# Performance work log

Measured on AMD Instinct MI355X. Metric: run time of the kernel, lower is better.

Reference implementation:

```python
import jax, jax.numpy as jnp
import numpy as np

HID = 128  # args['hidden_size']


def preprocess_adj(A):
    # A: [B, N, N] -> D^{-1/2} (A + I) D^{-1/2}
    N = A.shape[1]
    A_hat = A + jnp.eye(N, dtype=A.dtype)
    d = jnp.sum(A_hat, axis=2)                     # [B, N]
    d_safe = jnp.where(d > 0, d, 1.0)
    d_inv = jnp.where(d > 0, d_safe ** -0.5, 0.0)  # inf -> 0, as in torch code
    return d_inv[:, :, None] * A_hat * d_inv[:, None, :]


def lstm(x, w_ih, w_hh, b_ih, b_hh):
    # x: [B, T, H]; PyTorch gate order i, f, g, o; zero init state
    B = x.shape[0]
    H = w_hh.shape[1]
    def step(carry, xt):
        h, c = carry
        z = xt @ w_ih.T + b_ih + h @ w_hh.T + b_hh
        i, f, g, o = jnp.split(z, 4, axis=-1)
        c = jax.nn.sigmoid(f) * c + jax.nn.sigmoid(i) * jnp.tanh(g)
        h = jax.nn.sigmoid(o) * jnp.tanh(c)
        return (h, c), h
    h0 = jnp.zeros((B, H), x.dtype)
    c0 = jnp.zeros((B, H), x.dtype)
    _, hs = jax.lax.scan(step, (h0, c0), jnp.swapaxes(x, 0, 1))
    return jnp.swapaxes(hs, 0, 1)  # [B, T, H]


def gcn_dynamic_forward(x, A_norm, conv_w, conv_b, w_ih, w_hh, b_ih, b_hh):
    # x: [B, N, HID] with N >= HID: take last HID rows as dynamic-filter input
    df_in = x[:, x.shape[1] - HID:, :]              # [B, HID, HID]
    dyn = jax.lax.conv_general_dilated(
        df_in, conv_w, window_strides=(1,), padding=[(1, 1)],
        dimension_numbers=('NCH', 'OIH', 'NCH')) + conv_b[None, :, None]
    lw = lstm(dyn, w_ih, w_hh, b_ih, b_hh)          # [B, HID, HID]
    agg = jnp.matmul(A_norm, x)                     # [B, N, HID]
    out = jax.nn.sigmoid(jnp.matmul(agg, lw))       # output activation (1-layer GCN)
    return out                                       # dropout is identity in eval


def setup_inputs() -> dict:
    key = jax.random.key(0)
    ks = jax.random.split(key, 8)
    B, N = 4, 4096
    node_embedding = jax.random.normal(ks[0], (B, N, HID), dtype=jnp.float32)
    # sparse symmetric-ish 0/1 adjacency, avg degree ~ N*0.01
    adjacency_matrix = (jax.random.uniform(ks[1], (B, N, N)) < 0.01).astype(jnp.float32)
    s = 0.05
    conv_w = jax.random.normal(ks[2], (HID, HID, 3), dtype=jnp.float32) * s
    conv_b = jax.random.normal(ks[3], (HID,), dtype=jnp.float32) * s
    w_ih = jax.random.normal(ks[4], (4 * HID, HID), dtype=jnp.float32) * s
    w_hh = jax.random.normal(ks[5], (4 * HID, HID), dtype=jnp.float32) * s
    b_ih = jax.random.normal(ks[6], (4 * HID,), dtype=jnp.float32) * s
    b_hh = jax.random.normal(ks[7], (4 * HID,), dtype=jnp.float32) * s
    return {"node_embedding": node_embedding, "adjacency_matrix": adjacency_matrix,
            "conv_w": conv_w, "conv_b": conv_b,
            "w_ih": w_ih, "w_hh": w_hh, "b_ih": b_ih, "b_hh": b_hh}


def reference(node_embedding, adjacency_matrix, conv_w, conv_b, w_ih, w_hh, b_ih, b_hh):
    A_norm = preprocess_adj(adjacency_matrix)
    return gcn_dynamic_forward(node_embedding, A_norm, conv_w, conv_b, w_ih, w_hh, b_ih, b_hh)
```

## Files before the change

kernel.cpp:

```cpp
#include <hip/hip_runtime.h>
#include <math.h>

#define N_NODES 4096
#define HIDN 128
#define MAXNZ 128

typedef float v4f __attribute__((ext_vector_type(4)));
typedef _Float16 h2 __attribute__((ext_vector_type(2)));
typedef _Float16 h8 __attribute__((ext_vector_type(8)));

__device__ __forceinline__ float fsig(float x) { return 1.0f / (1.0f + __expf(-x)); }
__device__ __forceinline__ float ftanh_(float x) { return 1.0f - 2.0f / (__expf(2.0f * x) + 1.0f); }

__global__ __launch_bounds__(512) void k_conv(
        const float* __restrict__ x, const float* __restrict__ conv_w,
        const float* __restrict__ conv_b, const float* __restrict__ w_ih,
        const float* __restrict__ b_ih, const float* __restrict__ b_hh,
        float* __restrict__ z3) {
    const int cb = blockIdx.x;
    const int b = cb >> 5;
    const int t0 = (cb & 31) * 4;
    const int tsub = threadIdx.x >> 7;
    const int h = threadIdx.x & 127;
    const int t = t0 + tsub;
    __shared__ __align__(16) float dyn_lds[4][HIDN];
    const float* xb = x + ((size_t)b * N_NODES + (N_NODES - HIDN)) * HIDN;
    const float* w = conv_w + (size_t)t * HIDN * 3;
    float a0 = conv_b[t], a1 = 0.0f, a2 = 0.0f, a3 = 0.0f;
    #pragma unroll 4
    for (int i = 0; i < HIDN; i += 4) {
        const float* xr0 = xb + (size_t)i * HIDN;
        #pragma unroll
        for (int s = 0; s < 4; ++s) {
            const float* xr = xr0 + s * HIDN;
            float w0 = w[(i + s) * 3 + 0], w1 = w[(i + s) * 3 + 1], w2 = w[(i + s) * 3 + 2];
            float left  = (h > 0)   ? xr[h - 1] : 0.0f;
            float mid   = xr[h];
            float right = (h < 127) ? xr[h + 1] : 0.0f;
            if (s == 0)      a0 += left * w0 + mid * w1 + right * w2;
            else if (s == 1) a1 += left * w0 + mid * w1 + right * w2;
            else if (s == 2) a2 += left * w0 + mid * w1 + right * w2;
            else             a3 += left * w0 + mid * w1 + right * w2;
        }
    }
    dyn_lds[tsub][h] = (a0 + a1) + (a2 + a3);
    __syncthreads();
    const float4* dyn4 = (const float4*)dyn_lds[tsub];
    float* zrow = z3 + (size_t)(b * HIDN + t) * 512;
    for (int qg = 0; qg < 4; ++qg) {
        int u = h + 128 * qg;
        const float4* wr = (const float4*)(w_ih + (size_t)u * HIDN);
        float za = b_ih[u] + b_hh[u];
        #pragma unroll
        for (int f4 = 0; f4 < 32; ++f4) {
            float4 wv = wr[f4];
            float4 dv = dyn4[f4];
            za += wv.x * dv.x + wv.y * dv.y + wv.z * dv.z + wv.w * dv.w;
        }
        zrow[h * 4 + qg] = za;
    }
}

__global__ __launch_bounds__(512, 2) void k_lstm_scan(
        const float* __restrict__ z3, const float* __restrict__ w_hh,
        float* __restrict__ lw,
        const float* __restrict__ A, float* __restrict__ d_inv,
        int* __restrict__ cnt, int* __restrict__ idx) {
    if (blockIdx.x < 4) {
        const int b = blockIdx.x;
        const int t = threadIdx.x;
        const int m = t >> 2;
        const int q = t & 3;
        __shared__ __align__(16) h2 hbuf[2][64];
        h2 w2[4][16];
        #pragma unroll
        for (int g = 0; g < 4; ++g) {
            const float4* wr = (const float4*)(w_hh + ((size_t)(g * HIDN + m)) * HIDN + q * 32);
            #pragma unroll
            for (int j4 = 0; j4 < 8; ++j4) {
                float4 wv = wr[j4];
                w2[g][2 * j4 + 0] = h2{(_Float16)wv.x, (_Float16)wv.y};
                w2[g][2 * j4 + 1] = h2{(_Float16)wv.z, (_Float16)wv.w};
            }
        }
        float c = 0.0f;
        if (t < 64) hbuf[0][t] = h2{(_Float16)0.0f, (_Float16)0.0f};
        const float4* zb = (const float4*)z3 + (size_t)b * HIDN * HIDN;
        float4 zc = zb[0 * HIDN + m];
        float4 zn = zb[1 * HIDN + m];
        __syncthreads();
        for (int s = 0; s < HIDN; ++s) {
            const h8* hq8 = ((const h8*)hbuf[s & 1]) + q * 4;
            h8 H0 = hq8[0], H1 = hq8[1], H2 = hq8[2], H3 = hq8[3];
            const h2* hp = (const h2*)&H0;
            h2 hh[16];
            #pragma unroll
            for (int j = 0; j < 4; ++j) {
                hh[j]      = ((const h2*)&H0)[j];
                hh[4 + j]  = ((const h2*)&H1)[j];
                hh[8 + j]  = ((const h2*)&H2)[j];
                hh[12 + j] = ((const h2*)&H3)[j];
            }
            (void)hp;
            float s0a = 0.f, s0b = 0.f, s1a = 0.f, s1b = 0.f;
            float s2a = 0.f, s2b = 0.f, s3a = 0.f, s3b = 0.f;
            #pragma unroll
            for (int j = 0; j < 8; ++j) {
                s0a = __builtin_amdgcn_fdot2(w2[0][2 * j], hh[2 * j], s0a, false);
                s0b = __builtin_amdgcn_fdot2(w2[0][2 * j + 1], hh[2 * j + 1], s0b, false);
                s1a = __builtin_amdgcn_fdot2(w2[1][2 * j], hh[2 * j], s1a, false);
                s1b = __builtin_amdgcn_fdot2(w2[1][2 * j + 1], hh[2 * j + 1], s1b, false);
                s2a = __builtin_amdgcn_fdot2(w2[2][2 * j], hh[2 * j], s2a, false);
                s2b = __builtin_amdgcn_fdot2(w2[2][2 * j + 1], hh[2 * j + 1], s2b, false);
                s3a = __builtin_amdgcn_fdot2(w2[3][2 * j], hh[2 * j], s3a, false);
                s3b = __builtin_amdgcn_fdot2(w2[3][2 * j + 1], hh[2 * j + 1], s3b, false);
            }
            float z0 = s0a + s0b, z1 = s1a + s1b, z2 = s2a + s2b, z3s = s3a + s3b;
            z0 += __shfl_xor(z0, 1); z0 += __shfl_xor(z0, 2);
            z1 += __shfl_xor(z1, 1); z1 += __shfl_xor(z1, 2);
            z2 += __shfl_xor(z2, 1); z2 += __shfl_xor(z2, 2);
            z3s += __shfl_xor(z3s, 1); z3s += __shfl_xor(z3s, 2);
            z0 += zc.x; z1 += zc.y; z2 += zc.z; z3s += zc.w;
            float ig = fsig(z0);
            float fg = fsig(z1);
            float gg = ftanh_(z2);
            float og = fsig(z3s);
            c = fg * c + ig * gg;
            float hn = og * ftanh_(c);
            if (q == 0) {
                ((_Float16*)hbuf[(s + 1) & 1])[m] = (_Float16)hn;
                lw[(size_t)(b * HIDN + s) * HIDN + m] = hn;
            }
            zc = zn;
            int s2n = (s + 2 < HIDN) ? (s + 2) : (HIDN - 1);
            zn = zb[(size_t)s2n * HIDN + m];
            __syncthreads();
        }
    } else {
        const int wid = threadIdx.x >> 6;
        const int lane = threadIdx.x & 63;
        const int r = (blockIdx.x - 4) * 8 + wid;
        const v4f* row = (const v4f*)(A + (size_t)r * N_NODES);
        int* idx_row = idx + r * MAXNZ;
        const unsigned long long below = (1ull << lane) - 1ull;
        int cbase = 0;
#define PROC1(c, col)                                                         \
        {                                                                     \
            bool nz = ((c) != 0.0f);                                          \
            unsigned long long mm = __ballot(nz);                             \
            if (mm) {                                                         \
                if (nz) {                                                     \
                    int p_ = cbase + __popcll(mm & below);                    \
                    if (p_ < MAXNZ) idx_row[p_] = (col);                      \
                }                                                             \
                cbase += __popcll(mm);                                        \
            }                                                                 \
        }
        for (int half = 0; half < 2; ++half) {
            v4f v[8];
            #pragma unroll
            for (int j = 0; j < 8; ++j)
                v[j] = __builtin_nontemporal_load(&row[half * 512 + j * 64 + lane]);
            #pragma unroll
            for (int j = 0; j < 8; ++j) {
                int col0 = (half * 512 + j * 64 + lane) * 4;
                PROC1(v[j].x, col0 + 0);
                PROC1(v[j].y, col0 + 1);
                PROC1(v[j].z, col0 + 2);
                PROC1(v[j].w, col0 + 3);
            }
        }
#undef PROC1
        if (lane == 0) {
            cnt[r] = (cbase < MAXNZ) ? cbase : MAXNZ;
            d_inv[r] = rsqrtf((float)(cbase + 1));
        }
    }
}

__global__ __launch_bounds__(512) void k_gather(
        const float* __restrict__ x, const float* __restrict__ d_inv,
        const int* __restrict__ cnt, const int* __restrict__ idx,
        float* __restrict__ agg) {
    const int bIdx = blockIdx.x;
    const int b = (bIdx & 7) >> 1;
    const int o = ((bIdx >> 3) << 1) | (bIdx & 1);
    const int wid = threadIdx.x >> 6;
    const int lane = threadIdx.x & 63;
    __shared__ __align__(16) float dl[N_NODES];
    {
        const float4* dsrc = (const float4*)(d_inv + (b << 12));
        float4* ddst = (float4*)dl;
        ddst[threadIdx.x] = dsrc[threadIdx.x];
        ddst[threadIdx.x + 512] = dsrc[threadIdx.x + 512];
    }
    __syncthreads();
    const int i = o * 8 + wid;
    const int r = (b << 12) + i;
    const float2* xb = (const float2*)(x + (size_t)b * N_NODES * HIDN);
    const int4* irow4 = (const int4*)(idx + r * MAXNZ);
    const int n = cnt[r];
    float ax = 0.0f, ay = 0.0f;
    int k = 0;
    if (n >= 4) {
        int4 cur = irow4[0];
        for (; k + 4 <= n; k += 4) {
            int4 nxt = (k + 8 <= n) ? irow4[(k >> 2) + 1] : cur;
            float d0 = dl[cur.x], d1 = dl[cur.y], d2 = dl[cur.z], d3 = dl[cur.w];
            float2 v0 = xb[(size_t)cur.x * 64 + lane];
            float2 v1 = xb[(size_t)cur.y * 64 + lane];
            float2 v2 = xb[(size_t)cur.z * 64 + lane];
            float2 v3 = xb[(size_t)cur.w * 64 + lane];
            ax += d0 * v0.x + d1 * v1.x + d2 * v2.x + d3 * v3.x;
            ay += d0 * v0.y + d1 * v1.y + d2 * v2.y + d3 * v3.y;
            cur = nxt;
        }
    }
    const int* irow = (const int*)irow4;
    for (; k < n; ++k) {
        int j = irow[k];
        float dj = dl[j];
        float2 v = xb[(size_t)j * 64 + lane];
        ax += dj * v.x;
        ay += dj * v.y;
    }
    float di = dl[i];
    float2 vi = xb[(size_t)i * 64 + lane];
    float2 out;
    out.x = di * (ax + di * vi.x);
    out.y = di * (ay + di * vi.y);
    ((float2*)(agg + (size_t)r * HIDN))[lane] = out;
}

__global__ __launch_bounds__(256) void k_outmm(
        const float* __restrict__ agg, const float* __restrict__ lw,
        float* __restrict__ out) {
    __shared__ __align__(16) float lw_lds[HIDN * HIDN];
    const int i0 = blockIdx.x * 64;
    const int b = i0 >> 12;
    const float4* lwg = (const float4*)(lw + (size_t)b * HIDN * HIDN);
    float4* lds4 = (float4*)lw_lds;
    for (int v = threadIdx.x; v < HIDN * HIDN / 4; v += 256) lds4[v] = lwg[v];
    __syncthreads();
    const int r0 = i0 + (threadIdx.x >> 3) * 2;
    const int u0 = (threadIdx.x & 7) * 16;
    const float4* a4 = (const float4*)agg;
    float4 acc[2][4];
    #pragma unroll
    for (int rr = 0; rr < 2; ++rr)
        #pragma unroll
        for (int cc = 0; cc < 4; ++cc) acc[rr][cc] = make_float4(0.f, 0.f, 0.f, 0.f);
    for (int f4 = 0; f4 < 32; ++f4) {
        float4 a0 = a4[(size_t)r0 * 32 + f4];
        float4 a1 = a4[(size_t)(r0 + 1) * 32 + f4];
        #pragma unroll
        for (int ff = 0; ff < 4; ++ff) {
            float af0 = (ff == 0) ? a0.x : (ff == 1) ? a0.y : (ff == 2) ? a0.z : a0.w;
            float af1 = (ff == 0) ? a1.x : (ff == 1) ? a1.y : (ff == 2) ? a1.z : a1.w;
            int f = f4 * 4 + ff;
            const float4* wrow = (const float4*)(lw_lds + f * HIDN + u0);
            #pragma unroll
            for (int cc = 0; cc < 4; ++cc) {
                float4 wv = wrow[cc];
                acc[0][cc].x += af0 * wv.x; acc[0][cc].y += af0 * wv.y;
                acc[0][cc].z += af0 * wv.z; acc[0][cc].w += af0 * wv.w;
                acc[1][cc].x += af1 * wv.x; acc[1][cc].y += af1 * wv.y;
                acc[1][cc].z += af1 * wv.z; acc[1][cc].w += af1 * wv.w;
            }
        }
    }
    #pragma unroll
    for (int rr = 0; rr < 2; ++rr) {
        #pragma unroll
        for (int cc = 0; cc < 4; ++cc) {
            float4 ov;
            ov.x = fsig(acc[rr][cc].x);
            ov.y = fsig(acc[rr][cc].y);
            ov.z = fsig(acc[rr][cc].z);
            ov.w = fsig(acc[rr][cc].w);
            *(float4*)(out + (size_t)(r0 + rr) * HIDN + u0 + cc * 4) = ov;
        }
    }
}

extern "C" void kernel_launch(void* const* d_in, const int* in_sizes, int n_in,
                              void* d_out, int out_size, void* d_ws, size_t ws_size,
                              hipStream_t stream) {
    const float* x      = (const float*)d_in[0];
    const float* A      = (const float*)d_in[1];
    const float* conv_w = (const float*)d_in[2];
    const float* conv_b = (const float*)d_in[3];
    const float* w_ih   = (const float*)d_in[4];
    const float* w_hh   = (const float*)d_in[5];
    const float* b_ih   = (const float*)d_in[6];
    const float* b_hh   = (const float*)d_in[7];
    float* out = (float*)d_out;

    char* ws = (char*)d_ws;
    float* d_inv = (float*)ws;
    int*   cnt   = (int*)(ws + 65536);
    int*   idx   = (int*)(ws + 131072);
    float* z3    = (float*)(ws + 131072 + 8388608);
    float* lw    = (float*)(ws + 131072 + 8388608 + 1048576);
    float* agg   = (float*)(ws + 131072 + 8388608 + 1048576 + 262144);

    hipLaunchKernelGGL(k_conv, dim3(128), dim3(512), 0, stream,
                       x, conv_w, conv_b, w_ih, b_ih, b_hh, z3);
    hipLaunchKernelGGL(k_lstm_scan, dim3(2052), dim3(512), 0, stream,
                       z3, w_hh, lw, A, d_inv, cnt, idx);
    hipLaunchKernelGGL(k_gather, dim3(2048), dim3(512), 0, stream,
                       x, d_inv, cnt, idx, agg);
    hipLaunchKernelGGL(k_outmm, dim3(256), dim3(256), 0, stream, agg, lw, out);
}
```

Before: 573.2 us.

## Split LSTM and adjacency scan into separate kernels, chunk gate-input layout

Splits the combined kernel that ran the LSTM recurrence alongside the adjacency nonzero scan into two launches: k_scan, then k_lstm. The gate pre-activations are stored in 16-step chunks, so each thread loads its inputs per chunk with vector loads. Each thread folds its own gate input into a dot-product accumulator, and hidden states are buffered and written per chunk rather than every step. The gather kernel moves to 256-thread blocks with an 8-wide unrolled neighbour loop, and the scan drops its nontemporal loads. The cost is that the serial LSTM no longer overlaps the bandwidth-bound adjacency scan, so its latency lands on the critical path.

Result: slower. 606.9 us (+5.9%).

```diff
diff --git a/kernel.cpp b/kernel.cpp
--- a/kernel.cpp
+++ b/kernel.cpp
@@ -16,7 +16,7 @@
         const float* __restrict__ x, const float* __restrict__ conv_w,
         const float* __restrict__ conv_b, const float* __restrict__ w_ih,
         const float* __restrict__ b_ih, const float* __restrict__ b_hh,
-        float* __restrict__ z3) {
+        float* __restrict__ z4) {
     const int cb = blockIdx.x;
     const int b = cb >> 5;
     const int t0 = (cb & 31) * 4;
@@ -46,7 +46,7 @@
     dyn_lds[tsub][h] = (a0 + a1) + (a2 + a3);
     __syncthreads();
     const float4* dyn4 = (const float4*)dyn_lds[tsub];
-    float* zrow = z3 + (size_t)(b * HIDN + t) * 512;
+    const int ch = t >> 4, si = t & 15;
     for (int qg = 0; qg < 4; ++qg) {
         int u = h + 128 * qg;
         const float4* wr = (const float4*)(w_ih + (size_t)u * HIDN);
@@ -57,42 +57,86 @@
             float4 dv = dyn4[f4];
             za += wv.x * dv.x + wv.y * dv.y + wv.z * dv.z + wv.w * dv.w;
         }
-        zrow[h * 4 + qg] = za;
-    }
-}
-
-__global__ __launch_bounds__(512, 2) void k_lstm_scan(
-        const float* __restrict__ z3, const float* __restrict__ w_hh,
-        float* __restrict__ lw,
+        z4[(((size_t)(b * 8 + ch) * 128 + h) * 4 + qg) * 16 + si] = za;
+    }
+}
+
+__global__ __launch_bounds__(256) void k_scan(
         const float* __restrict__ A, float* __restrict__ d_inv,
         int* __restrict__ cnt, int* __restrict__ idx) {
-    if (blockIdx.x < 4) {
-        const int b = blockIdx.x;
-        const int t = threadIdx.x;
-        const int m = t >> 2;
-        const int q = t & 3;
-        __shared__ __align__(16) h2 hbuf[2][64];
-        h2 w2[4][16];
-        #pragma unroll
-        for (int g = 0; g < 4; ++g) {
-            const float4* wr = (const float4*)(w_hh + ((size_t)(g * HIDN + m)) * HIDN + q * 32);
-            #pragma unroll
-            for (int j4 = 0; j4 < 8; ++j4) {
-                float4 wv = wr[j4];
-                w2[g][2 * j4 + 0] = h2{(_Float16)wv.x, (_Float16)wv.y};
-                w2[g][2 * j4 + 1] = h2{(_Float16)wv.z, (_Float16)wv.w};
-            }
-        }
-        float c = 0.0f;
-        if (t < 64) hbuf[0][t] = h2{(_Float16)0.0f, (_Float16)0.0f};
-        const float4* zb = (const float4*)z3 + (size_t)b * HIDN * HIDN;
-        float4 zc = zb[0 * HIDN + m];
-        float4 zn = zb[1 * HIDN + m];
-        __syncthreads();
-        for (int s = 0; s < HIDN; ++s) {
+    const int wid = threadIdx.x >> 6;
+    const int lane = threadIdx.x & 63;
+    const int r = blockIdx.x * 4 + wid;
+    const v4f* row = (const v4f*)(A + (size_t)r * N_NODES);
+    int* idx_row = idx + r * MAXNZ;
+    const unsigned long long below = (1ull << lane) - 1ull;
+    int cbase = 0;
+#define PROC1(c, col)                                                         \
+    {                                                                         \
+        bool nz = ((c) != 0.0f);                                              \
+        unsigned long long mm = __ballot(nz);                                 \
+        if (mm) {                                                             \
+            if (nz) {                                                         \
+                int p_ = cbase + __popcll(mm & below);                        \
+                if (p_ < MAXNZ) idx_row[p_] = (col);                          \
+            }                                                                 \
+            cbase += __popcll(mm);                                            \
+        }                                                                     \
+    }
+    for (int half = 0; half < 2; ++half) {
+        v4f v[8];
+        #pragma unroll
+        for (int j = 0; j < 8; ++j)
+            v[j] = row[half * 512 + j * 64 + lane];
+        #pragma unroll
+        for (int j = 0; j < 8; ++j) {
+            int col0 = (half * 512 + j * 64 + lane) * 4;
+            PROC1(v[j].x, col0 + 0);
+            PROC1(v[j].y, col0 + 1);
+            PROC1(v[j].z, col0 + 2);
+            PROC1(v[j].w, col0 + 3);
+        }
+    }
+#undef PROC1
+    if (lane == 0) {
+        cnt[r] = (cbase < MAXNZ) ? cbase : MAXNZ;
+        d_inv[r] = rsqrtf((float)(cbase + 1));
+    }
+}
+
+__global__ __launch_bounds__(512) void k_lstm(
+        const float* __restrict__ z4, const float* __restrict__ w_hh,
+        float* __restrict__ lw) {
+    const int b = blockIdx.x;
+    const int t = threadIdx.x;
+    const int m = t >> 2;
+    const int q = t & 3;
+    __shared__ __align__(16) h2 hbuf[2][64];
+    h2 w2[4][16];
+    #pragma unroll
+    for (int g = 0; g < 4; ++g) {
+        const float4* wr = (const float4*)(w_hh + ((size_t)(g * HIDN + m)) * HIDN + q * 32);
+        #pragma unroll
+        for (int j4 = 0; j4 < 8; ++j4) {
+            float4 wv = wr[j4];
+            w2[g][2 * j4 + 0] = h2{(_Float16)wv.x, (_Float16)wv.y};
+            w2[g][2 * j4 + 1] = h2{(_Float16)wv.z, (_Float16)wv.w};
+        }
+    }
+    float c = 0.0f;
+    if (t < 64) hbuf[0][t] = h2{(_Float16)0.0f, (_Float16)0.0f};
+    __syncthreads();
+    for (int ch = 0; ch < 8; ++ch) {
+        const float4* zc = (const float4*)(z4 + ((((size_t)(b * 8 + ch) * 128 + m) * 4 + q) * 16));
+        float4 zr0 = zc[0], zr1 = zc[1], zr2 = zc[2], zr3 = zc[3];
+        float zs[16] = {zr0.x, zr0.y, zr0.z, zr0.w, zr1.x, zr1.y, zr1.z, zr1.w,
+                        zr2.x, zr2.y, zr2.z, zr2.w, zr3.x, zr3.y, zr3.z, zr3.w};
+        float hist[16];
+        #pragma unroll
+        for (int si = 0; si < 16; ++si) {
+            const int s = ch * 16 + si;
             const h8* hq8 = ((const h8*)hbuf[s & 1]) + q * 4;
             h8 H0 = hq8[0], H1 = hq8[1], H2 = hq8[2], H3 = hq8[3];
-            const h2* hp = (const h2*)&H0;
             h2 hh[16];
             #pragma unroll
             for (int j = 0; j < 4; ++j) {
@@ -101,84 +145,50 @@
                 hh[8 + j]  = ((const h2*)&H2)[j];
                 hh[12 + j] = ((const h2*)&H3)[j];
             }
-            (void)hp;
-            float s0a = 0.f, s0b = 0.f, s1a = 0.f, s1b = 0.f;
-            float s2a = 0.f, s2b = 0.f, s3a = 0.f, s3b = 0.f;
+            float zq = zs[si];
+            float a0 = (q == 0) ? zq : 0.0f, b0 = 0.0f;
+            float a1 = (q == 1) ? zq : 0.0f, b1 = 0.0f;
+            float a2 = (q == 2) ? zq : 0.0f, b2 = 0.0f;
+            float a3 = (q == 3) ? zq : 0.0f, b3 = 0.0f;
             #pragma unroll
             for (int j = 0; j < 8; ++j) {
-                s0a = __builtin_amdgcn_fdot2(w2[0][2 * j], hh[2 * j], s0a, false);
-                s0b = __builtin_amdgcn_fdot2(w2[0][2 * j + 1], hh[2 * j + 1], s0b, false);
-                s1a = __builtin_amdgcn_fdot2(w2[1][2 * j], hh[2 * j], s1a, false);
-                s1b = __builtin_amdgcn_fdot2(w2[1][2 * j + 1], hh[2 * j + 1], s1b, false);
-                s2a = __builtin_amdgcn_fdot2(w2[2][2 * j], hh[2 * j], s2a, false);
-                s2b = __builtin_amdgcn_fdot2(w2[2][2 * j + 1], hh[2 * j + 1], s2b, false);
-                s3a = __builtin_amdgcn_fdot2(w2[3][2 * j], hh[2 * j], s3a, false);
-                s3b = __builtin_amdgcn_fdot2(w2[3][2 * j + 1], hh[2 * j + 1], s3b, false);
+                a0 = __builtin_amdgcn_fdot2(w2[0][2 * j], hh[2 * j], a0, false);
+                b0 = __builtin_amdgcn_fdot2(w2[0][2 * j + 1], hh[2 * j + 1], b0, false);
+                a1 = __builtin_amdgcn_fdot2(w2[1][2 * j], hh[2 * j], a1, false);
+                b1 = __builtin_amdgcn_fdot2(w2[1][2 * j + 1], hh[2 * j + 1], b1, false);
+                a2 = __builtin_amdgcn_fdot2(w2[2][2 * j], hh[2 * j], a2, false);
+                b2 = __builtin_amdgcn_fdot2(w2[2][2 * j + 1], hh[2 * j + 1], b2, false);
+                a3 = __builtin_amdgcn_fdot2(w2[3][2 * j], hh[2 * j], a3, false);
+                b3 = __builtin_amdgcn_fdot2(w2[3][2 * j + 1], hh[2 * j + 1], b3, false);
             }
-            float z0 = s0a + s0b, z1 = s1a + s1b, z2 = s2a + s2b, z3s = s3a + s3b;
+            float z0 = a0 + b0, z1 = a1 + b1, z2 = a2 + b2, z3 = a3 + b3;
             z0 += __shfl_xor(z0, 1); z0 += __shfl_xor(z0, 2);
             z1 += __shfl_xor(z1, 1); z1 += __shfl_xor(z1, 2);
             z2 += __shfl_xor(z2, 1); z2 += __shfl_xor(z2, 2);
-            z3s += __shfl_xor(z3s, 1); z3s += __shfl_xor(z3s, 2);
-            z0 += zc.x; z1 += zc.y; z2 += zc.z; z3s += zc.w;
+            z3 += __shfl_xor(z3, 1); z3 += __shfl_xor(z3, 2);
             float ig = fsig(z0);
             float fg = fsig(z1);
             float gg = ftanh_(z2);
-            float og = fsig(z3s);
+            float og = fsig(z3);
             c = fg * c + ig * gg;
             float hn = og * ftanh_(c);
-            if (q == 0) {
-                ((_Float16*)hbuf[(s + 1) & 1])[m] = (_Float16)hn;
-                lw[(size_t)(b * HIDN + s) * HIDN + m] = hn;
+            hist[si] = hn;
+            if (q == 0) ((_Float16*)hbuf[(s + 1) & 1])[m] = (_Float16)hn;
+            __syncthreads();
+        }
+        float* lwb = lw + ((size_t)b * HIDN + ch * 16) * HIDN + m;
+        #pragma unroll
+        for (int qq = 0; qq < 4; ++qq) {
+            if (q == qq) {
+                #pragma unroll
+                for (int k = 0; k < 4; ++k)
+                    lwb[(size_t)(qq * 4 + k) * HIDN] = hist[qq * 4 + k];
             }
-            zc = zn;
-            int s2n = (s + 2 < HIDN) ? (s + 2) : (HIDN - 1);
-            zn = zb[(size_t)s2n * HIDN + m];
-            __syncthreads();
-        }
-    } else {
-        const int wid = threadIdx.x >> 6;
-        const int lane = threadIdx.x & 63;
-        const int r = (blockIdx.x - 4) * 8 + wid;
-        const v4f* row = (const v4f*)(A + (size_t)r * N_NODES);
-        int* idx_row = idx + r * MAXNZ;
-        const unsigned long long below = (1ull << lane) - 1ull;
-        int cbase = 0;
-#define PROC1(c, col)                                                         \
-        {                                                                     \
-            bool nz = ((c) != 0.0f);                                          \
-            unsigned long long mm = __ballot(nz);                             \
-            if (mm) {                                                         \
-                if (nz) {                                                     \
-                    int p_ = cbase + __popcll(mm & below);                    \
-                    if (p_ < MAXNZ) idx_row[p_] = (col);                      \
-                }                                                             \
-                cbase += __popcll(mm);                                        \
-            }                                                                 \
-        }
-        for (int half = 0; half < 2; ++half) {
-            v4f v[8];
-            #pragma unroll
-            for (int j = 0; j < 8; ++j)
-                v[j] = __builtin_nontemporal_load(&row[half * 512 + j * 64 + lane]);
-            #pragma unroll
-            for (int j = 0; j < 8; ++j) {
-                int col0 = (half * 512 + j * 64 + lane) * 4;
-                PROC1(v[j].x, col0 + 0);
-                PROC1(v[j].y, col0 + 1);
-                PROC1(v[j].z, col0 + 2);
-                PROC1(v[j].w, col0 + 3);
-            }
-        }
-#undef PROC1
-        if (lane == 0) {
-            cnt[r] = (cbase < MAXNZ) ? cbase : MAXNZ;
-            d_inv[r] = rsqrtf((float)(cbase + 1));
-        }
-    }
-}
-
-__global__ __launch_bounds__(512) void k_gather(
+        }
+    }
+}
+
+__global__ __launch_bounds__(256) void k_gather(
         const float* __restrict__ x, const float* __restrict__ d_inv,
         const int* __restrict__ cnt, const int* __restrict__ idx,
         float* __restrict__ agg) {
@@ -191,32 +201,36 @@
     {
         const float4* dsrc = (const float4*)(d_inv + (b << 12));
         float4* ddst = (float4*)dl;
-        ddst[threadIdx.x] = dsrc[threadIdx.x];
-        ddst[threadIdx.x + 512] = dsrc[threadIdx.x + 512];
+        #pragma unroll
+        for (int k = 0; k < 4; ++k)
+            ddst[threadIdx.x + 256 * k] = dsrc[threadIdx.x + 256 * k];
     }
     __syncthreads();
-    const int i = o * 8 + wid;
+    const int i = o * 4 + wid;
     const int r = (b << 12) + i;
     const float2* xb = (const float2*)(x + (size_t)b * N_NODES * HIDN);
-    const int4* irow4 = (const int4*)(idx + r * MAXNZ);
+    const int* irow = idx + r * MAXNZ;
     const int n = cnt[r];
     float ax = 0.0f, ay = 0.0f;
     int k = 0;
-    if (n >= 4) {
-        int4 cur = irow4[0];
-        for (; k + 4 <= n; k += 4) {
-            int4 nxt = (k + 8 <= n) ? irow4[(k >> 2) + 1] : cur;
-            float d0 = dl[cur.x], d1 = dl[cur.y], d2 = dl[cur.z], d3 = dl[cur.w];
-            float2 v0 = xb[(size_t)cur.x * 64 + lane];
-            float2 v1 = xb[(size_t)cur.y * 64 + lane];
-            float2 v2 = xb[(size_t)cur.z * 64 + lane];
-            float2 v3 = xb[(size_t)cur.w * 64 + lane];
-            ax += d0 * v0.x + d1 * v1.x + d2 * v2.x + d3 * v3.x;
-            ay += d0 * v0.y + d1 * v1.y + d2 * v2.y + d3 * v3.y;
-            cur = nxt;
-        }
-    }
-    const int* irow = (const int*)irow4;
+    for (; k + 8 <= n; k += 8) {
+        int4 j0 = *(const int4*)&irow[k];
+        int4 j1 = *(const int4*)&irow[k + 4];
+        float2 v0 = xb[(size_t)j0.x * 64 + lane];
+        float2 v1 = xb[(size_t)j0.y * 64 + lane];
+        float2 v2 = xb[(size_t)j0.z * 64 + lane];
+        float2 v3 = xb[(size_t)j0.w * 64 + lane];
+        float2 v4 = xb[(size_t)j1.x * 64 + lane];
+        float2 v5 = xb[(size_t)j1.y * 64 + lane];
+        float2 v6 = xb[(size_t)j1.z * 64 + lane];
+        float2 v7 = xb[(size_t)j1.w * 64 + lane];
+        float d0 = dl[j0.x], d1 = dl[j0.y], d2 = dl[j0.z], d3 = dl[j0.w];
+        float d4 = dl[j1.x], d5 = dl[j1.y], d6 = dl[j1.z], d7 = dl[j1.w];
+        ax += d0 * v0.x + d1 * v1.x + d2 * v2.x + d3 * v3.x
+            + d4 * v4.x + d5 * v5.x + d6 * v6.x + d7 * v7.x;
+        ay += d0 * v0.y + d1 * v1.y + d2 * v2.y + d3 * v3.y
+            + d4 * v4.y + d5 * v5.y + d6 * v6.y + d7 * v7.y;
+    }
     for (; k < n; ++k) {
         int j = irow[k];
         float dj = dl[j];
@@ -300,15 +314,16 @@
     float* d_inv = (float*)ws;
     int*   cnt   = (int*)(ws + 65536);
     int*   idx   = (int*)(ws + 131072);
-    float* z3    = (float*)(ws + 131072 + 8388608);
+    float* z4    = (float*)(ws + 131072 + 8388608);
     float* lw    = (float*)(ws + 131072 + 8388608 + 1048576);
     float* agg   = (float*)(ws + 131072 + 8388608 + 1048576 + 262144);
 
     hipLaunchKernelGGL(k_conv, dim3(128), dim3(512), 0, stream,
-                       x, conv_w, conv_b, w_ih, b_ih, b_hh, z3);
-    hipLaunchKernelGGL(k_lstm_scan, dim3(2052), dim3(512), 0, stream,
-                       z3, w_hh, lw, A, d_inv, cnt, idx);
-    hipLaunchKernelGGL(k_gather, dim3(2048), dim3(512), 0, stream,
+                       x, conv_w, conv_b, w_ih, b_ih, b_hh, z4);
+    hipLaunchKernelGGL(k_scan, dim3(4096), dim3(256), 0, stream,
+                       A, d_inv, cnt, idx);
+    hipLaunchKernelGGL(k_lstm, dim3(4), dim3(512), 0, stream, z4, w_hh, lw);
+    hipLaunchKernelGGL(k_gather, dim3(4096), dim3(256), 0, stream,
                        x, d_inv, cnt, idx, agg);
     hipLaunchKernelGGL(k_outmm, dim3(256), dim3(256), 0, stream, agg, lw, out);
 }
```
